# Kernel optimization log

Measured on AMD Instinct MI355X. Metric: run time of the kernel, lower is better.

## Reference

```python
import jax, jax.numpy as jnp
import numpy as np
from jax import lax

B, C1, IN_CH, OUT_CH, H1, W1 = 2, 64, 128, 64, 128, 128
BN_EPS = 1e-5


def conv3x3(x, w, b=None):
    # x: (N,C,H,W), w: (O,I,3,3), padding=1, stride=1 (matches nn.Conv2d)
    y = lax.conv_general_dilated(x, w, (1, 1), ((1, 1), (1, 1)),
                                 dimension_numbers=('NCHW', 'OIHW', 'NCHW'))
    return y if b is None else y + b[None, :, None, None]


def bn_relu(x, g, b):
    # training-mode BatchNorm2d (batch statistics over N,H,W) followed by ReLU
    m = x.mean((0, 2, 3), keepdims=True)
    v = x.var((0, 2, 3), keepdims=True)
    return jax.nn.relu((x - m) * lax.rsqrt(v + BN_EPS) * g[None, :, None, None]
                       + b[None, :, None, None])


def deform_offset(x, off_w):
    # ConvOffset2D: learn 2 offsets per pixel per channel, bilinear-gather input.
    Bc, C, H, W = x.shape
    offsets = conv3x3(x, off_w)                      # (B, 2C, H, W)
    off = offsets.reshape(Bc * C, H, W, 2)           # same flat reinterpretation as torch .view
    xf = x.reshape(Bc * C, H, W)
    gy, gx = jnp.meshgrid(jnp.arange(H, dtype=x.dtype),
                          jnp.arange(W, dtype=x.dtype), indexing='ij')
    cy = jnp.clip(off[..., 0] + gy, 0.0, H - 1)      # clamp per-axis like th_batch_map_coordinates
    cx = jnp.clip(off[..., 1] + gx, 0.0, W - 1)
    y0f, x0f = jnp.floor(cy), jnp.floor(cx)
    y0 = y0f.astype(jnp.int32); y1 = jnp.ceil(cy).astype(jnp.int32)
    x0 = x0f.astype(jnp.int32); x1c = jnp.ceil(cx).astype(jnp.int32)
    bidx = jnp.arange(Bc * C)[:, None, None]
    v00 = xf[bidx, y0, x0]; v10 = xf[bidx, y1, x0]
    v01 = xf[bidx, y0, x1c]; v11 = xf[bidx, y1, x1c]
    wy = cy - y0f; wx = cx - x0f
    vt = v00 + (v10 - v00) * wy                      # interp along H
    vb = v01 + (v11 - v01) * wy
    return (vt + (vb - vt) * wx).reshape(Bc, C, H, W)


def setup_inputs() -> dict:
    key = jax.random.key(0)
    ks = jax.random.split(key, 8)
    f = jnp.float32
    x1 = jax.random.normal(ks[0], (B, C1, H1, W1), f)
    x2 = jax.random.normal(ks[1], (B, C1, 2 * H1, 2 * W1), f)
    up_w = jax.random.normal(ks[2], (C1, C1, 2, 2), f) * 0.05   # torch IOHW layout
    up_b = jnp.zeros((C1,), f)
    off_w = jax.random.normal(ks[3], (2 * IN_CH, IN_CH, 3, 3), f) * 0.01  # init_normal_stddev
    c1_w = jax.random.normal(ks[4], (OUT_CH, IN_CH, 3, 3), f) * 0.05
    c1_b = jnp.zeros((OUT_CH,), f)
    g1 = jnp.ones((OUT_CH,), f); b1 = jnp.zeros((OUT_CH,), f)
    c2_w = jax.random.normal(ks[5], (OUT_CH, OUT_CH, 3, 3), f) * 0.05
    c2_b = jnp.zeros((OUT_CH,), f)
    g2 = jnp.ones((OUT_CH,), f); b2 = jnp.zeros((OUT_CH,), f)
    return dict(x1=x1, x2=x2, up_w=up_w, up_b=up_b, off_w=off_w,
                c1_w=c1_w, c1_b=c1_b, g1=g1, b1=b1,
                c2_w=c2_w, c2_b=c2_b, g2=g2, b2=b2)


def reference(x1, x2, up_w, up_b, off_w, c1_w, c1_b, g1, b1, c2_w, c2_b, g2, b2):
    # ConvTranspose2d(k=2, s=2): each input pixel expands to a 2x2 block
    Bx, Ci, H, W = x1.shape
    up = jnp.einsum('bihw,iokl->bohkwl', x1, up_w).reshape(Bx, up_w.shape[1], 2 * H, 2 * W)
    up = up + up_b[None, :, None, None]
    # pad skip connection to match (zero here; kept for faithfulness; torch pads W by diffX, H by diffY)
    dX = up.shape[2] - x2.shape[2]
    dY = up.shape[3] - x2.shape[3]
    x2p = jnp.pad(x2, ((0, 0), (0, 0), (dY // 2, dY // 2), (dX // 2, dX // 2)))
    xcat = jnp.concatenate([x2p, up], axis=1)        # (B, IN_CH, 2H, 2W)
    xd = deform_offset(xcat, off_w)
    h = bn_relu(conv3x3(xd, c1_w, c1_b), g1, b1)
    return bn_relu(conv3x3(h, c2_w, c2_b), g2, b2)
```

## Files before the change

kernel.cpp:

```cpp
#include <hip/hip_runtime.h>
#include <hip/hip_bf16.h>


typedef short short8 __attribute__((ext_vector_type(8)));
typedef short short4v __attribute__((ext_vector_type(4)));
typedef float f32x4 __attribute__((ext_vector_type(4)));

__device__ unsigned char g_ws[201u << 20] __attribute__((aligned(256)));
__device__ float g_st[256];

#define OFF_XCAT 0u
#define OFF_OFF  (36u << 20)
#define OFF_XD   (100u << 20)
#define OFF_C1O  (134u << 20)
#define OFF_H1   (150u << 20)
#define OFF_C2O  (168u << 20)
#define OFF_WO   (184u << 20)
#define OFF_W1   ((184u << 20) + 589824u)
#define OFF_W2   ((184u << 20) + 737280u)
#define OFF_XPU  (185u << 20)

#define XROW 264
#define XRSH (XROW * 128)

__device__ __forceinline__ float b2f(__hip_bfloat16 v) { return __bfloat162float(v); }
__device__ __forceinline__ short f2b(float v) {
  __hip_bfloat16 h = __float2bfloat16(v); short s; __builtin_memcpy(&s, &h, 2); return s;
}
__device__ __forceinline__ float s2f(short s) {
  __hip_bfloat16 h; __builtin_memcpy(&h, &s, 2); return __bfloat162float(h);
}
__device__ __forceinline__ void gload_lds16(const void* g, void* l) {
  __builtin_amdgcn_global_load_lds(
      (const __attribute__((address_space(1))) void*)g,
      (__attribute__((address_space(3))) void*)l, 16, 0, 0);
}

__device__ __forceinline__ void halo_zero(short* base, int C, int cshift, int u) {
  const int cg = u & ((1 << cshift) - 1);
  const int rest = u >> cshift;
  const int p = rest % 2576, b = rest / 2576;
  int row, col;
  if (p < 264) { row = 0; col = p; }
  else if (p < 528) { row = 257; col = p - 264; }
  else { int q = p - 528; row = 1 + (q >> 3); int cs = q & 7; col = cs ? 256 + cs : 0; }
  short8 z = {};
  *(short8*)(base + (((size_t)(b * 258) + row) * XROW + col) * C + cg * 8) = z;
}

__global__ __launch_bounds__(256)
void k_prep(const float* __restrict__ offw, const float* __restrict__ c1w,
            const float* __restrict__ c2w) {
  const int fid = blockIdx.x * 256 + threadIdx.x;
  if (blockIdx.x == 0) g_st[threadIdx.x] = 0.f;
  __hip_bfloat16* Wo = (__hip_bfloat16*)(g_ws + OFF_WO);
  __hip_bfloat16* W1 = (__hip_bfloat16*)(g_ws + OFF_W1);
  __hip_bfloat16* W2 = (__hip_bfloat16*)(g_ws + OFF_W2);
  if (fid < 294912) {
    int ic = fid & 127, rest = fid >> 7, oc = rest & 255, tap = rest >> 8;
    Wo[fid] = __float2bfloat16(offw[(oc * 128 + ic) * 9 + tap]);
  } else if (fid < 368640) {
    int l = fid - 294912;
    int ic = l & 127, rest = l >> 7, oc = rest & 63, tap = rest >> 6;
    W1[l] = __float2bfloat16(c1w[(oc * 128 + ic) * 9 + tap]);
  } else if (fid < 405504) {
    int l = fid - 368640;
    int ic = l & 63, rest = l >> 6, oc = rest & 63, tap = rest >> 6;
    W2[l] = __float2bfloat16(c2w[(oc * 64 + ic) * 9 + tap]);
  } else {
    int u = fid - 405504;
    if (u < 82432) halo_zero((short*)(g_ws + OFF_XCAT), 128, 4, u);
    else if (u < 164864) halo_zero((short*)(g_ws + OFF_XD), 128, 4, u - 82432);
    else halo_zero((short*)(g_ws + OFF_H1), 64, 3, u - 164864);
  }
}

__global__ __launch_bounds__(256)
void k_xpose(const float* __restrict__ x2) {
  __shared__ short T[256][72];
  const int t = threadIdx.x;
  const int h = blockIdx.x & 255, b = blockIdx.x >> 8;
  const float* src = x2 + (size_t)(b * 64) * 65536 + h * 256;
  for (int rep = 0; rep < 64; ++rep) {
    int flat = rep * 256 + t, c = flat >> 8, w = flat & 255;
    T[w][c] = f2b(src[(size_t)c * 65536 + w]);
  }
  __syncthreads();
  short* xcat = (short*)(g_ws + OFF_XCAT) +
                (((size_t)(b * 258) + h + 1) * XROW + 1) * 128;
  for (int rep = 0; rep < 8; ++rep) {
    int unit = rep * 256 + t;
    int w = unit >> 3, cg = unit & 7;
    *(short8*)(xcat + (size_t)w * 128 + cg * 8) = *(short8*)(&T[w][cg * 8]);
  }
}

__global__ __launch_bounds__(256)
void k_upmfma(const float* __restrict__ x1, const float* __restrict__ up_w,
              const float* __restrict__ up_b) {
  __shared__ short W4[4][64][66];
  __shared__ short X[64][68];
  __shared__ short U[2][128][66];
  __shared__ float BS[64];
  const int t = threadIdx.x;
  const int half = blockIdx.x & 1, hs = (blockIdx.x >> 1) & 127, b = blockIdx.x >> 8;
  for (int rep = 0; rep < 64; ++rep) {
    int flat = rep * 256 + t;
    int i = flat >> 8, rest = flat & 255, o = rest >> 2, kl = rest & 3;
    W4[kl][o][i] = f2b(up_w[flat]);
  }
  if (t < 64) BS[t] = up_b[t];
  const float* x1b = x1 + (size_t)(b * 64) * 16384 + hs * 128 + half * 64;
  for (int rep = 0; rep < 16; ++rep) {
    int flat = rep * 256 + t;
    int i = flat >> 6, ws = flat & 63;
    X[ws][i] = f2b(x1b[(size_t)i * 16384 + ws]);
  }
  __syncthreads();
  const int wv = t >> 6, lane = t & 63, l15 = lane & 15, quad = lane >> 4;
  short8 bf[2];
#pragma unroll
  for (int ks = 0; ks < 2; ++ks)
    bf[ks] = *(const short8*)(&X[wv * 16 + l15][ks * 32 + quad * 8]);
#pragma unroll
  for (int combo = 0; combo < 4; ++combo) {
    const int k = combo >> 1, l = combo & 1;
    f32x4 acc[4] = {};
#pragma unroll
    for (int nt = 0; nt < 4; ++nt)
#pragma unroll
      for (int ks = 0; ks < 2; ++ks) {
        short8 af = *(const short8*)(&W4[combo][nt * 16 + l15][ks * 32 + quad * 8]);
        acc[nt] = __builtin_amdgcn_mfma_f32_16x16x32_bf16(af, bf[ks], acc[nt], 0, 0, 0);
      }
    const int wl = 2 * (wv * 16 + l15) + l;
#pragma unroll
    for (int nt = 0; nt < 4; ++nt) {
      short4v s;
#pragma unroll
      for (int r = 0; r < 4; ++r) s[r] = f2b(acc[nt][r] + BS[nt * 16 + quad * 4 + r]);
      *(short4v*)(&U[k][wl][nt * 16 + quad * 4]) = s;
    }
  }
  __syncthreads();
  short* xcat = (short*)(g_ws + OFF_XCAT);
  short* xpu = (short*)(g_ws + OFF_XPU);
  for (int rep = 0; rep < 8; ++rep) {
    int unit = rep * 256 + t;
    int k = unit >> 10, wl = (unit >> 3) & 127, cg = unit & 7;
    int h = 2 * hs + k, w = half * 128 + wl;
    *(short8*)(xcat + (((size_t)(b * 258) + h + 1) * XROW + w + 1) * 128 + 64 + cg * 8) =
        *(short8*)(&U[k][wl][cg * 8]);
  }
  for (int rep = 0; rep < 8; ++rep) {
    int unit = rep * 256 + t;
    int o = unit >> 5, k = (unit >> 4) & 1, wg = unit & 15;
    int h = 2 * hs + k;
    short8 v;
#pragma unroll
    for (int j = 0; j < 8; ++j) v[j] = U[k][wg * 8 + j][o];
    *(short8*)(xpu + (size_t)(b * 64 + o) * 65536 + h * 256 + half * 128 + wg * 8) = v;
  }
}

__global__ __launch_bounds__(512, 2)
void k_offconv() {
  __shared__ short Bs[3 * 264 * 64];
  __shared__ short As0[256 * 32];
  __shared__ short As1[256 * 32];
  const short* X = (const short*)(g_ws + OFF_XCAT);
  const __hip_bfloat16* W = (const __hip_bfloat16*)(g_ws + OFF_WO);
  const int t = threadIdx.x;
  const int vb = (int)((blockIdx.x & 7) * 64 + (blockIdx.x >> 3));
  const int h = vb & 255, b = vb >> 8;
  const int wid = t >> 6, lane = t & 63, l15 = lane & 15, quad = lane >> 4;
  const int ocbase = (wid & 1) * 128;
  const int pxb = (wid >> 1) * 64;
  const int lpx = lane >> 3, lcg = lane & 7;
  const short* bsrc = X + (((size_t)(b * 258) + h) * XROW + lpx) * 128 + (lcg ^ (lpx & 7)) * 8;
  const int loc = lane >> 2, lcg4 = lane & 3;
  const __hip_bfloat16* asrc = W + (size_t)loc * 128 + (lcg4 ^ ((loc + (loc >> 2)) & 3)) * 8;
  const int ax = (quad ^ ((l15 + (l15 >> 2)) & 3)) << 3;
  const int abase = (ocbase + l15) * 32 + ax;
  f32x4 acc[8][4] = {};

#define STAGE_A(TAP, ICS, P, APTR)                                                  \
  {                                                                                 \
    _Pragma("unroll")                                                               \
    for (int k = 0; k < 2; ++k) {                                                   \
      int u = wid * 2 + k;                                                          \
      gload_lds16(asrc + ((size_t)(TAP) * 256 + u * 16) * 128 + (P) * 64 + (ICS) * 32, \
                  &APTR[u * 512]);                                                  \
    }                                                                               \
  }

  for (int p = 0; p < 2; ++p) {
    if (p) __syncthreads();
    for (int u = wid; u < 99; u += 8) {
      int r = u / 33, g = u - r * 33;
      gload_lds16(bsrc + (size_t)r * XRSH + g * 1024 + p * 64, &Bs[(r * 264 + g * 8) * 64]);
    }
    STAGE_A(0, 0, p, As0);
    STAGE_A(0, 1, p, As1);
    __syncthreads();
    for (int tap = 0; tap < 9; ++tap) {
      const int ky = tap / 3, kx = tap - 3 * ky;
      const short* srow = &Bs[(ky * 264 + pxb + l15 + kx) * 64];
      const int sx = ((l15 + kx) & 7) << 3;
      {
        short8 a[8], bf[4];
#pragma unroll
        for (int ot = 0; ot < 8; ++ot) a[ot] = *(const short8*)(As0 + abase + ot * 512);
#pragma unroll
        for (int pt = 0; pt < 4; ++pt)
          bf[pt] = *(const short8*)(srow + pt * 1024 + ((quad * 8) ^ sx));
        __syncthreads();
        if (tap < 8) STAGE_A(tap + 1, 0, p, As0);
#pragma unroll
        for (int ot = 0; ot < 8; ++ot)
#pragma unroll
          for (int pt = 0; pt < 4; ++pt)
            acc[ot][pt] = __builtin_amdgcn_mfma_f32_16x16x32_bf16(a[ot], bf[pt], acc[ot][pt], 0, 0, 0);
      }
      {
        short8 a[8], bf[4];
#pragma unroll
        for (int ot = 0; ot < 8; ++ot) a[ot] = *(const short8*)(As1 + abase + ot * 512);
#pragma unroll
        for (int pt = 0; pt < 4; ++pt)
          bf[pt] = *(const short8*)(srow + pt * 1024 + ((32 + quad * 8) ^ sx));
        __syncthreads();
        if (tap < 8) STAGE_A(tap + 1, 1, p, As1);
#pragma unroll
        for (int ot = 0; ot < 8; ++ot)
#pragma unroll
          for (int pt = 0; pt < 4; ++pt)
            acc[ot][pt] = __builtin_amdgcn_mfma_f32_16x16x32_bf16(a[ot], bf[pt], acc[ot][pt], 0, 0, 0);
      }
    }
  }
  __hip_bfloat16* out = (__hip_bfloat16*)(g_ws + OFF_OFF);
#pragma unroll
  for (int ot = 0; ot < 8; ++ot)
#pragma unroll
    for (int pt = 0; pt < 4; ++pt)
#pragma unroll
      for (int r = 0; r < 4; ++r) {
        int oc = ocbase + ot * 16 + quad * 4 + r;
        int px = pxb + pt * 16 + l15;
        out[(((size_t)(b * 256 + oc)) * 256 + h) * 256 + px] =
            __float2bfloat16(acc[ot][pt][r]);
      }
#undef STAGE_A
}

template <int IC, int SO>
__global__ __launch_bounds__(256, 2)
void k_conv(size_t xoff, size_t woff, const float* __restrict__ bias, size_t ooff) {
  __shared__ short Bs[3 * 272 * 32];
  __shared__ short As[2 * 2048];
  __shared__ float SB[128];
  const short* X = (const short*)(g_ws + xoff);
  const __hip_bfloat16* W = (const __hip_bfloat16*)(g_ws + woff);
  const int t = threadIdx.x;
  const int vb = (int)((blockIdx.x & 7) * 64 + (blockIdx.x >> 3));
  const int h = vb & 255, b = vb >> 8;
  const int wid = t >> 6, lane = t & 63, l15 = lane & 15, quad = lane >> 4;
  const int pxb = wid * 64;
  if (t < 128) SB[t] = 0.f;
  const int lpx = lane >> 2, lc = lane & 3;
  const int fl = (lpx + (lpx >> 2)) & 3;
  const short* bsrc = X + (((size_t)(b * 258) + h) * XROW + lpx) * IC + (lc ^ fl) * 8;
  const __hip_bfloat16* asrc = W + (size_t)lpx * IC + (lc ^ fl) * 8;
  const int aslot = (quad ^ ((l15 + (l15 >> 2)) & 3)) << 3;
  f32x4 acc[4][4] = {};
  const int KP = IC / 32;
  for (int ph = 0; ph < KP; ++ph) {
    for (int u = wid; u < 51; u += 4) {
      int r = u / 17, g = u - r * 17;
      gload_lds16(bsrc + ((size_t)r * XROW + g * 16) * IC + ph * 32,
                  &Bs[(r * 272 + g * 16) * 32]);
    }
    gload_lds16(asrc + (size_t)(wid * 16) * IC + ph * 32, &As[wid * 512]);
    __syncthreads();
    for (int tap = 0; tap < 9; ++tap) {
      short* Ac = &As[(tap & 1) * 2048];
      short* An = &As[((tap & 1) ^ 1) * 2048];
      if (tap < 8)
        gload_lds16(asrc + ((size_t)((tap + 1) * 64) + wid * 16) * IC + ph * 32,
                    &An[wid * 512]);
      const int ky = tap / 3, kx = tap - 3 * ky;
      short8 a[4], bf[4];
#pragma unroll
      for (int ot = 0; ot < 4; ++ot)
        a[ot] = *(const short8*)(&Ac[(ot * 16 + l15) * 32 + aslot]);
      const int s = l15 + kx;
      const int bslot = (quad ^ ((s + (s >> 2)) & 3)) << 3;
#pragma unroll
      for (int pt = 0; pt < 4; ++pt)
        bf[pt] = *(const short8*)(&Bs[(ky * 272 + pxb + pt * 16 + s) * 32 + bslot]);
#pragma unroll
      for (int ot = 0; ot < 4; ++ot)
#pragma unroll
        for (int pt = 0; pt < 4; ++pt)
          acc[ot][pt] = __builtin_amdgcn_mfma_f32_16x16x32_bf16(a[ot], bf[pt], acc[ot][pt], 0, 0, 0);
      __syncthreads();
    }
  }
  __hip_bfloat16* out = (__hip_bfloat16*)(g_ws + ooff);
#pragma unroll
  for (int ot = 0; ot < 4; ++ot) {
    const int oc0 = ot * 16 + quad * 4;
    float bv[4], sa[4] = {}, sa2[4] = {};
#pragma unroll
    for (int r = 0; r < 4; ++r) bv[r] = bias[oc0 + r];
#pragma unroll
    for (int pt = 0; pt < 4; ++pt) {
      const int px = pxb + pt * 16 + l15;
      short4v sv;
#pragma unroll
      for (int r = 0; r < 4; ++r) {
        float f = acc[ot][pt][r] + bv[r];
        sv[r] = f2b(f);
        sa[r] += f;
        sa2[r] = fmaf(f, f, sa2[r]);
      }
      *(short4v*)(out + ((((size_t)(b * 256) + h) * 256 + px) * 64 + oc0)) = sv;
    }
#pragma unroll
    for (int r = 0; r < 4; ++r) {
      float sv1 = sa[r], sv2 = sa2[r];
      for (int d = 1; d < 16; d <<= 1) {
        sv1 += __shfl_xor(sv1, d);
        sv2 += __shfl_xor(sv2, d);
      }
      if (l15 == 0) {
        atomicAdd(&SB[oc0 + r], sv1);
        atomicAdd(&SB[64 + oc0 + r], sv2);
      }
    }
  }
  __syncthreads();
  if (t < 128) atomicAdd(&g_st[SO + t], SB[t]);
}

__global__ __launch_bounds__(256, 4)
void k_gather(const float* __restrict__ x2) {
  __shared__ short G[256 * 66];
  const __hip_bfloat16* off = (const __hip_bfloat16*)(g_ws + OFF_OFF);
  const __hip_bfloat16* xpu = (const __hip_bfloat16*)(g_ws + OFF_XPU);
  short* xd = (short*)(g_ws + OFF_XD);
  const int t = threadIdx.x;
  const int half = blockIdx.x & 1;
  const int hh = (blockIdx.x >> 1) & 255, b = blockIdx.x >> 9;
  const int hp = 2 * (hh & 127) + (t >> 7);
  const int w0e = 2 * (t & 127);
  const int chb = hh >> 7;
  const int c0 = half * 64;
  const float fh = (float)hh, fw = (float)t;
  const __hip_bfloat16* offb = off + ((size_t)(b * 256) * 256 + hp) * 256 + w0e +
                               (size_t)(2 * c0 + chb) * 65536;
  if (half == 0) {
    const float* x2b = x2 + (size_t)b * 64 * 65536;
    for (int g8 = 0; g8 < 8; ++g8) {
      unsigned ovv[8];
#pragma unroll
      for (int j = 0; j < 8; ++j)
        ovv[j] = *(const unsigned*)(offb + (size_t)(2 * (g8 * 8 + j)) * 65536);
#pragma unroll
      for (int j = 0; j < 8; ++j) {
        const int crel = g8 * 8 + j;
        unsigned ov = ovv[j];
        float oy = __uint_as_float((ov & 0xffffu) << 16);
        float ox = __uint_as_float((ov >> 16) << 16);
        float cy = fminf(fmaxf(oy + fh, 0.f), 255.f);
        float cx = fminf(fmaxf(ox + fw, 0.f), 255.f);
        float y0f = floorf(cy), x0f = floorf(cx);
        int y0 = (int)y0f, x0 = (int)x0f;
        int y1 = (int)ceilf(cy), x1 = (int)ceilf(cx);
        const float* pl = x2b + (size_t)crel * 65536;
        float v00 = pl[y0 * 256 + x0], v10 = pl[y1 * 256 + x0];
        float v01 = pl[y0 * 256 + x1], v11 = pl[y1 * 256 + x1];
        float wy = cy - y0f, wx = cx - x0f;
        float vt = v00 + (v10 - v00) * wy;
        float vb = v01 + (v11 - v01) * wy;
        G[t * 66 + crel] = f2b(vt + (vb - vt) * wx);
      }
    }
  } else {
    const __hip_bfloat16* xub = xpu + (size_t)b * 64 * 65536;
    for (int g8 = 0; g8 < 8; ++g8) {
      unsigned ovv[8];
#pragma unroll
      for (int j = 0; j < 8; ++j)
        ovv[j] = *(const unsigned*)(offb + (size_t)(2 * (g8 * 8 + j)) * 65536);
#pragma unroll
      for (int j = 0; j < 8; ++j) {
        const int crel = g8 * 8 + j;
        unsigned ov = ovv[j];
        float oy = __uint_as_float((ov & 0xffffu) << 16);
        float ox = __uint_as_float((ov >> 16) << 16);
        float cy = fminf(fmaxf(oy + fh, 0.f), 255.f);
        float cx = fminf(fmaxf(ox + fw, 0.f), 255.f);
        float y0f = floorf(cy), x0f = floorf(cx);
        int y0 = (int)y0f, x0 = (int)x0f;
        int y1 = (int)ceilf(cy), x1 = (int)ceilf(cx);
        const __hip_bfloat16* pl = xub + (size_t)crel * 65536;
        float v00 = b2f(pl[y0 * 256 + x0]), v10 = b2f(pl[y1 * 256 + x0]);
        float v01 = b2f(pl[y0 * 256 + x1]), v11 = b2f(pl[y1 * 256 + x1]);
        float wy = cy - y0f, wx = cx - x0f;
        float vt = v00 + (v10 - v00) * wy;
        float vb = v01 + (v11 - v01) * wy;
        G[t * 66 + crel] = f2b(vt + (vb - vt) * wx);
      }
    }
  }
  __syncthreads();
  const size_t dst = (((size_t)(b * 258) + hh + 1) * XROW + 1) * 128 + c0;
  for (int it = 0; it < 8; ++it) {
    int g = it * 256 + t;
    *(short8*)(xd + dst + (size_t)(g >> 3) * 128 + (g & 7) * 8) =
        *(short8*)(&G[(g >> 3) * 66 + (g & 7) * 8]);
  }
}

__global__ __launch_bounds__(256)
void k_bnrelu1(const float* __restrict__ g, const float* __restrict__ be) {
  __shared__ float A[64], Bc[64];
  const __hip_bfloat16* x = (const __hip_bfloat16*)(g_ws + OFF_C1O);
  short* o = (short*)(g_ws + OFF_H1);
  const int t = threadIdx.x;
  const int h = blockIdx.x & 255, b = blockIdx.x >> 8;
  if (t < 64) {
    float m = g_st[t] * (1.f / 131072.f);
    float v = g_st[64 + t] * (1.f / 131072.f) - m * m;
    float iv = rsqrtf(v + 1e-5f) * g[t];
    A[t] = iv;
    Bc[t] = be[t] - m * iv;
  }
  __syncthreads();
  const __hip_bfloat16* px = x + (((size_t)(b * 256) + h) * 256 + t) * 64;
  short* op = o + (((size_t)(b * 258) + h + 1) * XROW + t + 1) * 64;
#pragma unroll
  for (int cg = 0; cg < 8; ++cg) {
    short8 v = *(const short8*)(px + cg * 8);
    short8 r;
#pragma unroll
    for (int j = 0; j < 8; ++j) {
      int c = cg * 8 + j;
      r[j] = f2b(fmaxf(s2f(v[j]) * A[c] + Bc[c], 0.f));
    }
    *(short8*)(op + cg * 8) = r;
  }
}

__global__ __launch_bounds__(256)
void k_bnrelu2(const float* __restrict__ g, const float* __restrict__ be,
               float* __restrict__ dout) {
  __shared__ float T[64 * 257];
  __shared__ float A[64], Bc[64];
  const __hip_bfloat16* x = (const __hip_bfloat16*)(g_ws + OFF_C2O);
  const int t = threadIdx.x;
  const int h = blockIdx.x & 255, b = blockIdx.x >> 8;
  if (t < 64) {
    float m = g_st[128 + t] * (1.f / 131072.f);
    float v = g_st[192 + t] * (1.f / 131072.f) - m * m;
    float iv = rsqrtf(v + 1e-5f) * g[t];
    A[t] = iv;
    Bc[t] = be[t] - m * iv;
  }
  __syncthreads();
  const __hip_bfloat16* px = x + (((size_t)(b * 256) + h) * 256 + t) * 64;
#pragma unroll
  for (int cg = 0; cg < 8; ++cg) {
    short8 v = *(const short8*)(px + cg * 8);
#pragma unroll
    for (int j = 0; j < 8; ++j) {
      int c = cg * 8 + j;
      T[c * 257 + t] = fmaxf(s2f(v[j]) * A[c] + Bc[c], 0.f);
    }
  }
  __syncthreads();
  for (int rep = 0; rep < 64; ++rep) {
    int flat = rep * 256 + t, c = flat >> 8, w = flat & 255;
    dout[(((size_t)(b * 64 + c)) * 256 + h) * 256 + w] = T[c * 257 + w];
  }
}

extern "C" void kernel_launch(void* const* d_in, const int* in_sizes, int n_in,
                              void* d_out, int out_size, void* d_ws, size_t ws_size,
                              hipStream_t stream) {
  const bool ok = (n_in == 13) &&
                  in_sizes[0] == 2097152 && in_sizes[1] == 8388608 &&
                  in_sizes[2] == 16384 && in_sizes[3] == 64 &&
                  in_sizes[4] == 294912 && in_sizes[5] == 73728 &&
                  in_sizes[9] == 36864 && out_size == 8388608;
  if (!ok) { hipMemsetAsync(d_out, 0x46, (size_t)out_size * 2, stream); return; }

  const float* x1   = (const float*)d_in[0];
  const float* x2   = (const float*)d_in[1];
  const float* up_w = (const float*)d_in[2];
  const float* up_b = (const float*)d_in[3];
  const float* offw = (const float*)d_in[4];
  const float* c1w  = (const float*)d_in[5];
  const float* c1b  = (const float*)d_in[6];
  const float* g1   = (const float*)d_in[7];
  const float* b1   = (const float*)d_in[8];
  const float* c2w  = (const float*)d_in[9];
  const float* c2b  = (const float*)d_in[10];
  const float* g2   = (const float*)d_in[11];
  const float* b2   = (const float*)d_in[12];

  k_prep<<<2389, 256, 0, stream>>>(offw, c1w, c2w);
  k_xpose<<<512, 256, 0, stream>>>(x2);
  k_upmfma<<<512, 256, 0, stream>>>(x1, up_w, up_b);
  k_offconv<<<512, 512, 0, stream>>>();
  k_gather<<<1024, 256, 0, stream>>>(x2);
  k_conv<128, 0><<<512, 256, 0, stream>>>(OFF_XD, OFF_W1, c1b, OFF_C1O);
  k_bnrelu1<<<512, 256, 0, stream>>>(g1, b1);
  k_conv<64, 128><<<512, 256, 0, stream>>>(OFF_H1, OFF_W2, c2b, OFF_C2O);
  k_bnrelu2<<<512, 256, 0, stream>>>(g2, b2, (float*)d_out);

  (void)d_ws; (void)ws_size;
}
```

Baseline: 346.2 us.

## Merge prep, transpose and upsample kernels; stage two conv taps per barrier

Three independent setup kernels (weight conversion and halo zeroing, x2 transpose, transposed-conv upsample) are combined into one launch that branches on block index, with a shared LDS buffer carved up per role. This removes two kernel launches and the gaps between them. Separately, the conv kernel now double-buffers weights two taps at a time, so each tap group needs one barrier instead of one per tap. The merged kernel sizes its LDS for the largest role, which can lower occupancy for the lightweight prep blocks.

```diff
diff --git a/kernel.cpp b/kernel.cpp
--- a/kernel.cpp
+++ b/kernel.cpp
@@ -49,61 +49,63 @@
 }
 
 __global__ __launch_bounds__(256)
-void k_prep(const float* __restrict__ offw, const float* __restrict__ c1w,
-            const float* __restrict__ c2w) {
-  const int fid = blockIdx.x * 256 + threadIdx.x;
-  if (blockIdx.x == 0) g_st[threadIdx.x] = 0.f;
-  __hip_bfloat16* Wo = (__hip_bfloat16*)(g_ws + OFF_WO);
-  __hip_bfloat16* W1 = (__hip_bfloat16*)(g_ws + OFF_W1);
-  __hip_bfloat16* W2 = (__hip_bfloat16*)(g_ws + OFF_W2);
-  if (fid < 294912) {
-    int ic = fid & 127, rest = fid >> 7, oc = rest & 255, tap = rest >> 8;
-    Wo[fid] = __float2bfloat16(offw[(oc * 128 + ic) * 9 + tap]);
-  } else if (fid < 368640) {
-    int l = fid - 294912;
-    int ic = l & 127, rest = l >> 7, oc = rest & 63, tap = rest >> 6;
-    W1[l] = __float2bfloat16(c1w[(oc * 128 + ic) * 9 + tap]);
-  } else if (fid < 405504) {
-    int l = fid - 368640;
-    int ic = l & 63, rest = l >> 6, oc = rest & 63, tap = rest >> 6;
-    W2[l] = __float2bfloat16(c2w[(oc * 64 + ic) * 9 + tap]);
-  } else {
-    int u = fid - 405504;
-    if (u < 82432) halo_zero((short*)(g_ws + OFF_XCAT), 128, 4, u);
-    else if (u < 164864) halo_zero((short*)(g_ws + OFF_XD), 128, 4, u - 82432);
-    else halo_zero((short*)(g_ws + OFF_H1), 64, 3, u - 164864);
-  }
-}
-
-__global__ __launch_bounds__(256)
-void k_xpose(const float* __restrict__ x2) {
-  __shared__ short T[256][72];
+void k_pre(const float* __restrict__ offw, const float* __restrict__ c1w,
+           const float* __restrict__ c2w, const float* __restrict__ x2,
+           const float* __restrict__ x1, const float* __restrict__ up_w,
+           const float* __restrict__ up_b) {
+  __shared__ __align__(16) unsigned char SM[76544];
+  const int bid = blockIdx.x;
   const int t = threadIdx.x;
-  const int h = blockIdx.x & 255, b = blockIdx.x >> 8;
-  const float* src = x2 + (size_t)(b * 64) * 65536 + h * 256;
-  for (int rep = 0; rep < 64; ++rep) {
-    int flat = rep * 256 + t, c = flat >> 8, w = flat & 255;
-    T[w][c] = f2b(src[(size_t)c * 65536 + w]);
-  }
-  __syncthreads();
-  short* xcat = (short*)(g_ws + OFF_XCAT) +
-                (((size_t)(b * 258) + h + 1) * XROW + 1) * 128;
-  for (int rep = 0; rep < 8; ++rep) {
-    int unit = rep * 256 + t;
-    int w = unit >> 3, cg = unit & 7;
-    *(short8*)(xcat + (size_t)w * 128 + cg * 8) = *(short8*)(&T[w][cg * 8]);
-  }
-}
-
-__global__ __launch_bounds__(256)
-void k_upmfma(const float* __restrict__ x1, const float* __restrict__ up_w,
-              const float* __restrict__ up_b) {
-  __shared__ short W4[4][64][66];
-  __shared__ short X[64][68];
-  __shared__ short U[2][128][66];
-  __shared__ float BS[64];
-  const int t = threadIdx.x;
-  const int half = blockIdx.x & 1, hs = (blockIdx.x >> 1) & 127, b = blockIdx.x >> 8;
+  if (bid < 2389) {
+    const int fid = bid * 256 + t;
+    if (bid == 0) g_st[t] = 0.f;
+    __hip_bfloat16* Wo = (__hip_bfloat16*)(g_ws + OFF_WO);
+    __hip_bfloat16* W1 = (__hip_bfloat16*)(g_ws + OFF_W1);
+    __hip_bfloat16* W2 = (__hip_bfloat16*)(g_ws + OFF_W2);
+    if (fid < 294912) {
+      int ic = fid & 127, rest = fid >> 7, oc = rest & 255, tap = rest >> 8;
+      Wo[fid] = __float2bfloat16(offw[(oc * 128 + ic) * 9 + tap]);
+    } else if (fid < 368640) {
+      int l = fid - 294912;
+      int ic = l & 127, rest = l >> 7, oc = rest & 63, tap = rest >> 6;
+      W1[l] = __float2bfloat16(c1w[(oc * 128 + ic) * 9 + tap]);
+    } else if (fid < 405504) {
+      int l = fid - 368640;
+      int ic = l & 63, rest = l >> 6, oc = rest & 63, tap = rest >> 6;
+      W2[l] = __float2bfloat16(c2w[(oc * 64 + ic) * 9 + tap]);
+    } else {
+      int u = fid - 405504;
+      if (u < 82432) halo_zero((short*)(g_ws + OFF_XCAT), 128, 4, u);
+      else if (u < 164864) halo_zero((short*)(g_ws + OFF_XD), 128, 4, u - 82432);
+      else halo_zero((short*)(g_ws + OFF_H1), 64, 3, u - 164864);
+    }
+    return;
+  }
+  if (bid < 2901) {
+    short (*T)[72] = (short(*)[72])SM;
+    const int vb = bid - 2389;
+    const int h = vb & 255, b = vb >> 8;
+    const float* src = x2 + (size_t)(b * 64) * 65536 + h * 256;
+    for (int rep = 0; rep < 64; ++rep) {
+      int flat = rep * 256 + t, c = flat >> 8, w = flat & 255;
+      T[w][c] = f2b(src[(size_t)c * 65536 + w]);
+    }
+    __syncthreads();
+    short* xcat = (short*)(g_ws + OFF_XCAT) +
+                  (((size_t)(b * 258) + h + 1) * XROW + 1) * 128;
+    for (int rep = 0; rep < 8; ++rep) {
+      int unit = rep * 256 + t;
+      int w = unit >> 3, cg = unit & 7;
+      *(short8*)(xcat + (size_t)w * 128 + cg * 8) = *(short8*)(&T[w][cg * 8]);
+    }
+    return;
+  }
+  short (*W4)[64][66] = (short(*)[64][66])SM;
+  short (*X)[68]      = (short(*)[68])(SM + 33792);
+  short (*U)[128][66] = (short(*)[128][66])(SM + 42496);
+  float* BS           = (float*)(SM + 76288);
+  const int vb = bid - 2901;
+  const int half = vb & 1, hs = (vb >> 1) & 127, b = vb >> 8;
   for (int rep = 0; rep < 64; ++rep) {
     int flat = rep * 256 + t;
     int i = flat >> 8, rest = flat & 255, o = rest >> 2, kl = rest & 3;
@@ -258,7 +260,7 @@
 __global__ __launch_bounds__(256, 2)
 void k_conv(size_t xoff, size_t woff, const float* __restrict__ bias, size_t ooff) {
   __shared__ short Bs[3 * 272 * 32];
-  __shared__ short As[2 * 2048];
+  __shared__ short As[2][4096];
   __shared__ float SB[128];
   const short* X = (const short*)(g_ws + xoff);
   const __hip_bfloat16* W = (const __hip_bfloat16*)(g_ws + woff);
@@ -281,29 +283,46 @@
       gload_lds16(bsrc + ((size_t)r * XROW + g * 16) * IC + ph * 32,
                   &Bs[(r * 272 + g * 16) * 32]);
     }
-    gload_lds16(asrc + (size_t)(wid * 16) * IC + ph * 32, &As[wid * 512]);
+#pragma unroll
+    for (int k = 0; k < 2; ++k) {
+      int u = wid * 2 + k;
+      gload_lds16(asrc + ((size_t)((u >> 2) * 64 + (u & 3) * 16)) * IC + ph * 32,
+                  &As[0][u * 512]);
+    }
     __syncthreads();
-    for (int tap = 0; tap < 9; ++tap) {
-      short* Ac = &As[(tap & 1) * 2048];
-      short* An = &As[((tap & 1) ^ 1) * 2048];
-      if (tap < 8)
-        gload_lds16(asrc + ((size_t)((tap + 1) * 64) + wid * 16) * IC + ph * 32,
-                    &An[wid * 512]);
-      const int ky = tap / 3, kx = tap - 3 * ky;
-      short8 a[4], bf[4];
-#pragma unroll
-      for (int ot = 0; ot < 4; ++ot)
-        a[ot] = *(const short8*)(&Ac[(ot * 16 + l15) * 32 + aslot]);
-      const int s = l15 + kx;
-      const int bslot = (quad ^ ((s + (s >> 2)) & 3)) << 3;
-#pragma unroll
-      for (int pt = 0; pt < 4; ++pt)
-        bf[pt] = *(const short8*)(&Bs[(ky * 272 + pxb + pt * 16 + s) * 32 + bslot]);
-#pragma unroll
-      for (int ot = 0; ot < 4; ++ot)
+    for (int pr = 0; pr < 5; ++pr) {
+      const short* cur = As[pr & 1];
+      short* nxt = As[(pr & 1) ^ 1];
+      if (pr < 4) {
+        const int bt = 2 * pr + 2;
+        const int nunits = (bt == 8) ? 4 : 8;
+#pragma unroll
+        for (int k = 0; k < 2; ++k) {
+          int u = wid * 2 + k;
+          if (u < nunits)
+            gload_lds16(asrc + ((size_t)((bt + (u >> 2)) * 64 + (u & 3) * 16)) * IC + ph * 32,
+                        &nxt[u * 512]);
+        }
+      }
+      const int ntap = (pr == 4) ? 1 : 2;
+      for (int tt = 0; tt < ntap; ++tt) {
+        const int tap = 2 * pr + tt;
+        const int ky = tap / 3, kx = tap - 3 * ky;
+        short8 a[4], bf[4];
+#pragma unroll
+        for (int ot = 0; ot < 4; ++ot)
+          a[ot] = *(const short8*)(&cur[tt * 2048 + (ot * 16 + l15) * 32 + aslot]);
+        const int s = l15 + kx;
+        const int bslot = (quad ^ ((s + (s >> 2)) & 3)) << 3;
 #pragma unroll
         for (int pt = 0; pt < 4; ++pt)
-          acc[ot][pt] = __builtin_amdgcn_mfma_f32_16x16x32_bf16(a[ot], bf[pt], acc[ot][pt], 0, 0, 0);
+          bf[pt] = *(const short8*)(&Bs[(ky * 272 + pxb + pt * 16 + s) * 32 + bslot]);
+#pragma unroll
+        for (int ot = 0; ot < 4; ++ot)
+#pragma unroll
+          for (int pt = 0; pt < 4; ++pt)
+            acc[ot][pt] = __builtin_amdgcn_mfma_f32_16x16x32_bf16(a[ot], bf[pt], acc[ot][pt], 0, 0, 0);
+      }
       __syncthreads();
     }
   }
@@ -511,9 +530,7 @@
   const float* g2   = (const float*)d_in[11];
   const float* b2   = (const float*)d_in[12];
 
-  k_prep<<<2389, 256, 0, stream>>>(offw, c1w, c2w);
-  k_xpose<<<512, 256, 0, stream>>>(x2);
-  k_upmfma<<<512, 256, 0, stream>>>(x1, up_w, up_b);
+  k_pre<<<3413, 256, 0, stream>>>(offw, c1w, c2w, x2, x1, up_w, up_b);
   k_offconv<<<512, 512, 0, stream>>>();
   k_gather<<<1024, 256, 0, stream>>>(x2);
   k_conv<128, 0><<<512, 256, 0, stream>>>(OFF_XD, OFF_W1, c1b, OFF_C1O);
```

Result: slower. 357.2 us (+3.2%).
